# Kernel tuning notes

Measured on AMD Instinct MI355X. Metric: run time of the kernel, lower is better.

## Reference

```python
import jax, jax.numpy as jnp
import numpy as np

N_EMBD = 1024
N_HEAD = 16
HEAD_DIM = N_EMBD // N_HEAD
B, T = 2, 2048


def setup_inputs() -> dict:
    key = jax.random.key(0)
    ks = jax.random.split(key, 12)
    s = 0.02
    inp = {
        "x": jax.random.normal(ks[0], (B, T, N_EMBD), dtype=jnp.float32),
        "ln1_g": jnp.ones((N_EMBD,), jnp.float32),
        "ln1_b": jnp.zeros((N_EMBD,), jnp.float32),
        "ln2_g": jnp.ones((N_EMBD,), jnp.float32),
        "ln2_b": jnp.zeros((N_EMBD,), jnp.float32),
        "W_qkv": jax.random.normal(ks[1], (N_EMBD, 3 * N_EMBD), jnp.float32) * s,
        "b_qkv": jnp.zeros((3 * N_EMBD,), jnp.float32),
        "W_o": jax.random.normal(ks[2], (N_EMBD, N_EMBD), jnp.float32) * s,
        "b_o": jnp.zeros((N_EMBD,), jnp.float32),
        "W_fc": jax.random.normal(ks[3], (N_EMBD, 4 * N_EMBD), jnp.float32) * s,
        "b_fc": jnp.zeros((4 * N_EMBD,), jnp.float32),
        "W_proj": jax.random.normal(ks[4], (4 * N_EMBD, N_EMBD), jnp.float32) * s,
        "b_proj": jnp.zeros((N_EMBD,), jnp.float32),
    }
    return inp


def _layernorm(x, g, b, eps=1e-5):
    mu = jnp.mean(x, axis=-1, keepdims=True)
    var = jnp.var(x, axis=-1, keepdims=True)
    return (x - mu) * jax.lax.rsqrt(var + eps) * g + b


def _block(x, ln1_g, ln1_b, ln2_g, ln2_b, W_qkv, b_qkv, W_o, b_o, W_fc, b_fc, W_proj, b_proj):
    # --- attention sub-block (pre-LN) ---
    h = _layernorm(x, ln1_g, ln1_b)
    qkv = h @ W_qkv + b_qkv                     # [B,T,3E]
    q, k, v = jnp.split(qkv, 3, axis=-1)
    def split_heads(t):
        return t.reshape(B, T, N_HEAD, HEAD_DIM).transpose(0, 2, 1, 3)  # [B,H,T,D]
    q, k, v = split_heads(q), split_heads(k), split_heads(v)
    scores = jnp.einsum("bhqd,bhkd->bhqk", q, k) / (HEAD_DIM ** 0.5)
    causal = jnp.tril(jnp.ones((T, T), dtype=bool))
    scores = jnp.where(causal, scores, jnp.float32(-jnp.inf))
    probs = jax.nn.softmax(scores, axis=-1)
    attn = jnp.einsum("bhqk,bhkd->bhqd", probs, v)        # [B,H,T,D]
    attn = attn.transpose(0, 2, 1, 3).reshape(B, T, N_EMBD)
    x = x + attn @ W_o + b_o
    # --- MLP sub-block (pre-LN) ---
    h = _layernorm(x, ln2_g, ln2_b)
    h = jax.nn.gelu(h @ W_fc + b_fc, approximate=False)
    x = x + h @ W_proj + b_proj
    return x


def reference(x, ln1_g, ln1_b, ln2_g, ln2_b, W_qkv, b_qkv, W_o, b_o, W_fc, b_fc, W_proj, b_proj):
    return _block(x, ln1_g, ln1_b, ln2_g, ln2_b, W_qkv, b_qkv, W_o, b_o, W_fc, b_fc, W_proj, b_proj)
```

## Files before the change

### kernel.cpp

```cpp
#include <hip/hip_runtime.h>
#include <hip/hip_bf16.h>


#define TT 2048
#define EE 1024
#define NH 16
#define HD 64

#define AS1 __attribute__((address_space(1)))
#define AS3 __attribute__((address_space(3)))

using bf16x8 = __bf16 __attribute__((ext_vector_type(8)));
using bf16x4 = __bf16 __attribute__((ext_vector_type(4)));
using f32x4  = float __attribute__((ext_vector_type(4)));

template<int N> __device__ __forceinline__ void vm_wait() {
    if constexpr (N == 0)      asm volatile("s_waitcnt vmcnt(0)" ::: "memory");
    else if constexpr (N == 3) asm volatile("s_waitcnt vmcnt(3)" ::: "memory");
    else                       asm volatile("s_waitcnt vmcnt(4)" ::: "memory");
}

__device__ __forceinline__ float gelu_fast(float v) {
    float z  = v * 0.70710678118f;
    float az = fabsf(z);
    float t  = __builtin_amdgcn_rcpf(__builtin_fmaf(0.3275911f, az, 1.0f));
    float p  = t * __builtin_fmaf(t,
                   __builtin_fmaf(t,
                     __builtin_fmaf(t,
                       __builtin_fmaf(t, 1.061405429f, -1.453152027f),
                       1.421413741f),
                     -0.284496736f),
                   0.254829592f);
    float e  = __expf(-az * az);
    float er = copysignf(1.0f - p * e, z);
    return 0.5f * v * (1.0f + er);
}

__global__ __launch_bounds__(256) void convt_kernel(const float* __restrict__ W,
                                                    __bf16* __restrict__ WT,
                                                    int K, int N) {
    __shared__ __bf16 t[32][33];
    int n0 = blockIdx.x * 32, k0 = blockIdx.y * 32;
    int tid = threadIdx.x;
    int r = tid >> 3, c4 = (tid & 7) * 4;
    float4 v = *(const float4*)(W + (size_t)(k0 + r) * N + n0 + c4);
    t[r][c4 + 0] = (__bf16)v.x; t[r][c4 + 1] = (__bf16)v.y;
    t[r][c4 + 2] = (__bf16)v.z; t[r][c4 + 3] = (__bf16)v.w;
    __syncthreads();
    bf16x4 o;
    o[0] = t[c4 + 0][r]; o[1] = t[c4 + 1][r];
    o[2] = t[c4 + 2][r]; o[3] = t[c4 + 3][r];
    *(bf16x4*)(WT + (size_t)(n0 + r) * K + k0 + c4) = o;
}

__global__ __launch_bounds__(256) void ln_kernel(const float* __restrict__ x,
                                                 const float* __restrict__ g,
                                                 const float* __restrict__ bta,
                                                 __bf16* __restrict__ out) {
    int row = blockIdx.x;
    int tid = threadIdx.x;
    const float4 xv = *(const float4*)(x + (size_t)row * EE + tid * 4);
    float s  = xv.x + xv.y + xv.z + xv.w;
    float ss = xv.x*xv.x + xv.y*xv.y + xv.z*xv.z + xv.w*xv.w;
    __shared__ float rs[256], rss[256];
    rs[tid] = s; rss[tid] = ss;
    __syncthreads();
    for (int st = 128; st > 0; st >>= 1) {
        if (tid < st) { rs[tid] += rs[tid+st]; rss[tid] += rss[tid+st]; }
        __syncthreads();
    }
    float mean = rs[0] * (1.0f / EE);
    float var  = rss[0] * (1.0f / EE) - mean * mean;
    float rstd = rsqrtf(var + 1e-5f);
    const float4 gv = *(const float4*)(g + tid * 4);
    const float4 bv = *(const float4*)(bta + tid * 4);
    bf16x4 ov;
    ov[0] = (__bf16)((xv.x - mean) * rstd * gv.x + bv.x);
    ov[1] = (__bf16)((xv.y - mean) * rstd * gv.y + bv.y);
    ov[2] = (__bf16)((xv.z - mean) * rstd * gv.z + bv.z);
    ov[3] = (__bf16)((xv.w - mean) * rstd * gv.w + bv.w);
    *(bf16x4*)(out + (size_t)row * EE + tid * 4) = ov;
}

template<int TM, int TN, bool GELU, bool RESID, bool QKV, typename CT>
__global__ __launch_bounds__(256) void gemm_bt_kernel(const __bf16* __restrict__ A,
                                                      const __bf16* __restrict__ BT,
                                                      const float* __restrict__ bias,
                                                      const float* resid, CT* C,
                                                      __bf16* vT,
                                                      int M, int N, int K) {
    constexpr int MT = TM / 32;
    constexpr int NT = TN / 32;
    constexpr int LOADS = TM / 64 + TN / 64;
    __shared__ __align__(16) __bf16 As[3][TM][32];
    __shared__ __align__(16) __bf16 Bs[3][TN][32];
    int tid = threadIdx.x, wave = tid >> 6, lane = tid & 63;
    int quad = lane >> 4, l16 = lane & 15;
    int wm = wave >> 1, wn = wave & 1;
    int m0 = blockIdx.y * TM, n0 = blockIdx.x * TN;

    f32x4 acc[MT][NT] = {};

    int srow = wave * 16 + (lane >> 2);
    int scol = (lane & 3) * 8;

    auto STAGE = [&](int buf, int kt) {
        int kb = kt << 5;
#pragma unroll
        for (int p = 0; p < TM / 64; p++) {
            const __bf16* g = A + (size_t)(m0 + p * 64 + srow) * K + kb + scol;
            __builtin_amdgcn_global_load_lds((AS1 const void*)g,
                                             (AS3 void*)&As[buf][p * 64 + wave * 16][0],
                                             16, 0, 0);
        }
#pragma unroll
        for (int p = 0; p < TN / 64; p++) {
            const __bf16* g = BT + (size_t)(n0 + p * 64 + srow) * K + kb + scol;
            __builtin_amdgcn_global_load_lds((AS1 const void*)g,
                                             (AS3 void*)&Bs[buf][p * 64 + wave * 16][0],
                                             16, 0, 0);
        }
    };

    const int nk = K >> 5;
    STAGE(0, 0);
    STAGE(1, 1);
    vm_wait<LOADS>();
    __builtin_amdgcn_s_barrier();

    for (int t = 0; t < nk; ++t) {
        const int cur = t % 3;
        if (t + 2 < nk) STAGE((t + 2) % 3, t + 2);

        bf16x8 af[MT], bfr[NT];
#pragma unroll
        for (int mt = 0; mt < MT; mt++)
            af[mt] = *(const bf16x8*)(&As[cur][wm * (MT * 16) + mt * 16 + l16][quad * 8]);
#pragma unroll
        for (int nt = 0; nt < NT; nt++)
            bfr[nt] = *(const bf16x8*)(&Bs[cur][wn * (NT * 16) + nt * 16 + l16][quad * 8]);
#pragma unroll
        for (int mt = 0; mt < MT; mt++)
#pragma unroll
            for (int nt = 0; nt < NT; nt++)
                acc[mt][nt] = __builtin_amdgcn_mfma_f32_16x16x32_bf16(af[mt], bfr[nt],
                                                                      acc[mt][nt], 0, 0, 0);
        if (t + 1 < nk) {
            if (t + 2 < nk) vm_wait<LOADS>();
            else            vm_wait<0>();
            __builtin_amdgcn_s_barrier();
        }
    }

#pragma unroll
    for (int nt = 0; nt < NT; nt++) {
        int c = n0 + wn * (NT * 16) + nt * 16 + l16;
        float bv = bias[c];
#pragma unroll
        for (int mt = 0; mt < MT; mt++) {
#pragma unroll
            for (int r = 0; r < 4; r++) {
                int row = m0 + wm * (MT * 16) + mt * 16 + quad * 4 + r;
                float v = acc[mt][nt][r] + bv;
                if (GELU)  v = gelu_fast(v);
                if (RESID) v += resid[(size_t)row * N + c];
                if (!QKV) {
                    C[(size_t)row * N + c] = (CT)v;
                } else {
                    if (c < 2 * EE) {
                        ((__bf16*)C)[(size_t)row * (2 * EE) + c] = (__bf16)v;
                    } else {
                        int cv = c - 2 * EE;
                        int bb = row >> 11, t = row & (TT - 1);
                        vT[((size_t)(bb * NH + (cv >> 6)) * HD + (cv & 63)) * TT + t] =
                            (__bf16)v;
                    }
                }
            }
        }
    }
}

__global__ __launch_bounds__(256) void flash_attn_kernel(const __bf16* __restrict__ qkv,
                                                         const __bf16* __restrict__ vT,
                                                         __bf16* __restrict__ out) {
    int h = blockIdx.y, b = blockIdx.z;
    int tid = threadIdx.x, wave = tid >> 6, lane = tid & 63;
    int quad = lane >> 4, l16 = lane & 15;

    __shared__ __align__(16) __bf16 Ks[128 * 72];
    __shared__ __align__(16) __bf16 Ps[4][16 * 136];

    size_t base = (size_t)b * TT * (2 * EE);

    int srow = tid >> 3;
    int scol = (tid & 7) * 8;
    const __bf16* kbase  = qkv + base + EE + h * HD + scol;
    const __bf16* vrow = vT + (size_t)(b * NH + h) * HD * TT + (size_t)l16 * TT + quad * 8;
    __bf16* Psw = &Ps[wave][0];

    int nTiles = (int)gridDim.x * 2;

    for (int pass = 0; pass < 2; pass++) {
        int qt = pass == 0 ? (nTiles - 1 - blockIdx.x) : blockIdx.x;
        int q0 = qt * 64;

        int qrow = q0 + wave * 16 + l16;
        const __bf16* qp = qkv + base + (size_t)qrow * (2 * EE) + h * HD;
        bf16x8 aq0 = *(const bf16x8*)(qp + quad * 8);
        bf16x8 aq1 = *(const bf16x8*)(qp + 32 + quad * 8);

        f32x4 oacc[4] = {};
        float lsum[4] = {0.f, 0.f, 0.f, 0.f};
        int qg_base = q0 + wave * 16 + quad * 4;

        int nIter = (qt >> 1) + 1;

        bf16x8 kr[4];
#pragma unroll
        for (int p = 0; p < 4; p++)
            kr[p] = *(const bf16x8*)(kbase + (size_t)(32 * p + srow) * (2 * EE));

        for (int kt = 0; kt < nIter; ++kt) {
            int k0 = kt * 128;
#pragma unroll
            for (int p = 0; p < 4; p++)
                *(bf16x8*)(&Ks[(32 * p + srow) * 72 + scol]) = kr[p];
            __syncthreads();

            bf16x8 vf[4][4];
#pragma unroll
            for (int dt = 0; dt < 4; dt++)
#pragma unroll
                for (int w = 0; w < 4; w++)
                    vf[dt][w] = *(const bf16x8*)(vrow + (size_t)dt * (16 * TT) + k0 + w * 32);

            if (kt < nIter - 1) {
                int kn = k0 + 128;
#pragma unroll
                for (int p = 0; p < 4; p++)
                    kr[p] = *(const bf16x8*)(kbase + (size_t)(kn + 32 * p + srow) * (2 * EE));
            }

            f32x4 s[8];
#pragma unroll
            for (int nt = 0; nt < 8; nt++) {
                bf16x8 bk0 = *(const bf16x8*)(&Ks[(nt * 16 + l16) * 72 + quad * 8]);
                bf16x8 bk1 = *(const bf16x8*)(&Ks[(nt * 16 + l16) * 72 + 32 + quad * 8]);
                f32x4 z = {};
                z = __builtin_amdgcn_mfma_f32_16x16x32_bf16(aq0, bk0, z, 0, 0, 0);
                s[nt] = __builtin_amdgcn_mfma_f32_16x16x32_bf16(aq1, bk1, z, 0, 0, 0);
            }

            bool maskt = (kt == nIter - 1);
#pragma unroll
            for (int nt = 0; nt < 8; nt++) {
                int key = k0 + nt * 16 + l16;
                int cb = 2 * nt + (l16 >> 3);
#pragma unroll
                for (int r = 0; r < 4; r++) {
                    float p;
                    if (maskt && key > qg_base + r) p = 0.0f;
                    else p = __expf(fminf(s[nt][r] * 0.125f, 30.0f));
                    lsum[r] += p;
                    int q = quad * 4 + r;
                    int col = (((cb & 8) | ((cb - 2 * q) & 7)) << 3) | (l16 & 7);
                    Psw[q * 136 + col] = (__bf16)p;
                }
            }

#pragma unroll
            for (int w = 0; w < 4; w++) {
                int cbr = 4 * w + quad;
                int colr = ((cbr & 8) | ((cbr - 2 * l16) & 7)) << 3;
                bf16x8 ap = *(const bf16x8*)(&Psw[l16 * 136 + colr]);
#pragma unroll
                for (int dt = 0; dt < 4; dt++)
                    oacc[dt] = __builtin_amdgcn_mfma_f32_16x16x32_bf16(ap, vf[dt][w],
                                                                       oacc[dt], 0, 0, 0);
            }
            __syncthreads();
        }

#pragma unroll
        for (int off = 1; off < 16; off <<= 1)
#pragma unroll
            for (int r = 0; r < 4; r++) lsum[r] += __shfl_xor(lsum[r], off);
#pragma unroll
        for (int dt = 0; dt < 4; dt++) {
#pragma unroll
            for (int r = 0; r < 4; r++) {
                int qg = qg_base + r;
                out[((size_t)b * TT + qg) * EE + h * HD + dt * 16 + l16] =
                    (__bf16)(oacc[dt][r] / lsum[r]);
            }
        }
    }
}

extern "C" void kernel_launch(void* const* d_in, const int* in_sizes, int n_in,
                              void* d_out, int out_size, void* d_ws, size_t ws_size,
                              hipStream_t stream) {
    const float* x     = (const float*)d_in[0];
    const float* ln1g  = (const float*)d_in[1];
    const float* ln1b  = (const float*)d_in[2];
    const float* ln2g  = (const float*)d_in[3];
    const float* ln2b  = (const float*)d_in[4];
    const float* Wqkv  = (const float*)d_in[5];
    const float* bqkv  = (const float*)d_in[6];
    const float* Wo    = (const float*)d_in[7];
    const float* bo    = (const float*)d_in[8];
    const float* Wfc   = (const float*)d_in[9];
    const float* bfc   = (const float*)d_in[10];
    const float* Wproj = (const float*)d_in[11];
    const float* bproj = (const float*)d_in[12];
    float* out = (float*)d_out;

    const int M = 2 * TT;

    __bf16* ws = (__bf16*)d_ws;
    __bf16* regQ   = ws;
    __bf16* regS   = ws + 16777216;
    __bf16* WfcT   = ws + 20971520;
    __bf16* qkv    = regQ;
    __bf16* vT     = regQ + 8388608;
    __bf16* WqkvT  = regQ + 12582912;
    __bf16* WoT    = regQ + 15728640;
    __bf16* ff     = regQ;
    __bf16* h1 = regS, *atn = regS, *h2 = regS;
    __bf16* WprojT = regS;
    float*  x1 = out;

    convt_kernel<<<dim3(3 * EE / 32, EE / 32), 256, 0, stream>>>(Wqkv, WqkvT, EE, 3 * EE);
    convt_kernel<<<dim3(EE / 32, EE / 32), 256, 0, stream>>>(Wo, WoT, EE, EE);
    convt_kernel<<<dim3(4 * EE / 32, EE / 32), 256, 0, stream>>>(Wfc, WfcT, EE, 4 * EE);

    ln_kernel<<<M, 256, 0, stream>>>(x, ln1g, ln1b, h1);
    gemm_bt_kernel<128, 128, false, false, true, __bf16>
        <<<dim3(3 * EE / 128, M / 128), 256, 0, stream>>>(
        h1, WqkvT, bqkv, nullptr, qkv, vT, M, 3 * EE, EE);
    flash_attn_kernel<<<dim3(TT / 128, NH, 2), 256, 0, stream>>>(qkv, vT, atn);
    gemm_bt_kernel<128, 64, false, true, false, float>
        <<<dim3(EE / 64, M / 128), 256, 0, stream>>>(
        atn, WoT, bo, x, x1, nullptr, M, EE, EE);
    ln_kernel<<<M, 256, 0, stream>>>(x1, ln2g, ln2b, h2);
    gemm_bt_kernel<128, 128, true, false, false, __bf16>
        <<<dim3(4 * EE / 128, M / 128), 256, 0, stream>>>(
        h2, WfcT, bfc, nullptr, ff, nullptr, M, 4 * EE, EE);
    convt_kernel<<<dim3(EE / 32, 4 * EE / 32), 256, 0, stream>>>(Wproj, WprojT, 4 * EE, EE);
    gemm_bt_kernel<128, 64, false, true, false, float>
        <<<dim3(EE / 64, M / 128), 256, 0, stream>>>(
        ff, WprojT, bproj, x1, out, nullptr, M, EE, 4 * EE);
}
```

Measured before the change: 429.3 us.

## Deepen GEMM LDS pipeline to four stages and XOR-swizzle LDS tiles

The bf16 GEMM kernel now uses four shared-memory buffers, prefetching three k-tiles ahead, whenever each stage issues three or fewer loads. The vmcnt wait thresholds are derived from the pipeline depth, and a separate tail loop drains the remaining tiles. Global-to-LDS copies and the fragment reads now use a matching XOR swizzle on the 16-byte column chunk, meant to reduce LDS bank conflicts on the bf16x8 reads. The extra buffer raises LDS use per block, which may lower occupancy.

```diff
diff --git a/kernel.cpp b/kernel.cpp
--- a/kernel.cpp
+++ b/kernel.cpp
@@ -16,8 +16,11 @@
 
 template<int N> __device__ __forceinline__ void vm_wait() {
     if constexpr (N == 0)      asm volatile("s_waitcnt vmcnt(0)" ::: "memory");
+    else if constexpr (N == 2) asm volatile("s_waitcnt vmcnt(2)" ::: "memory");
     else if constexpr (N == 3) asm volatile("s_waitcnt vmcnt(3)" ::: "memory");
-    else                       asm volatile("s_waitcnt vmcnt(4)" ::: "memory");
+    else if constexpr (N == 4) asm volatile("s_waitcnt vmcnt(4)" ::: "memory");
+    else if constexpr (N == 6) asm volatile("s_waitcnt vmcnt(6)" ::: "memory");
+    else                       asm volatile("s_waitcnt vmcnt(8)" ::: "memory");
 }
 
 __device__ __forceinline__ float gelu_fast(float v) {
@@ -92,8 +95,11 @@
     constexpr int MT = TM / 32;
     constexpr int NT = TN / 32;
     constexpr int LOADS = TM / 64 + TN / 64;
-    __shared__ __align__(16) __bf16 As[3][TM][32];
-    __shared__ __align__(16) __bf16 Bs[3][TN][32];
+    constexpr int NBUF  = (LOADS <= 3) ? 4 : 3;
+    constexpr int DEPTH = NBUF - 1;
+    constexpr int WAITN = (DEPTH - 1) * LOADS;
+    __shared__ __align__(16) __bf16 As[NBUF][TM][32];
+    __shared__ __align__(16) __bf16 Bs[NBUF][TN][32];
     int tid = threadIdx.x, wave = tid >> 6, lane = tid & 63;
     int quad = lane >> 4, l16 = lane & 15;
     int wm = wave >> 1, wn = wave & 1;
@@ -102,7 +108,8 @@
     f32x4 acc[MT][NT] = {};
 
     int srow = wave * 16 + (lane >> 2);
-    int scol = (lane & 3) * 8;
+    int scol = (((lane & 3) ^ ((lane >> 3) & 3)) * 8);
+    int xcol = ((quad ^ ((l16 >> 1) & 3)) * 8);
 
     auto STAGE = [&](int buf, int kt) {
         int kb = kt << 5;
@@ -122,32 +129,41 @@
         }
     };
 
-    const int nk = K >> 5;
-    STAGE(0, 0);
-    STAGE(1, 1);
-    vm_wait<LOADS>();
-    __builtin_amdgcn_s_barrier();
-
-    for (int t = 0; t < nk; ++t) {
-        const int cur = t % 3;
-        if (t + 2 < nk) STAGE((t + 2) % 3, t + 2);
-
+    auto COMPUTE = [&](int cur) {
         bf16x8 af[MT], bfr[NT];
 #pragma unroll
         for (int mt = 0; mt < MT; mt++)
-            af[mt] = *(const bf16x8*)(&As[cur][wm * (MT * 16) + mt * 16 + l16][quad * 8]);
+            af[mt] = *(const bf16x8*)(&As[cur][wm * (MT * 16) + mt * 16 + l16][xcol]);
 #pragma unroll
         for (int nt = 0; nt < NT; nt++)
-            bfr[nt] = *(const bf16x8*)(&Bs[cur][wn * (NT * 16) + nt * 16 + l16][quad * 8]);
+            bfr[nt] = *(const bf16x8*)(&Bs[cur][wn * (NT * 16) + nt * 16 + l16][xcol]);
 #pragma unroll
         for (int mt = 0; mt < MT; mt++)
 #pragma unroll
             for (int nt = 0; nt < NT; nt++)
                 acc[mt][nt] = __builtin_amdgcn_mfma_f32_16x16x32_bf16(af[mt], bfr[nt],
                                                                       acc[mt][nt], 0, 0, 0);
+    };
+
+    const int nk = K >> 5;
+#pragma unroll
+    for (int i = 0; i < DEPTH; ++i) STAGE(i, i);
+    vm_wait<WAITN>();
+    __builtin_amdgcn_s_barrier();
+
+    int t = 0;
+    for (; t + DEPTH < nk; ++t) {
+        STAGE((t + DEPTH) % NBUF, t + DEPTH);
+        COMPUTE(t % NBUF);
+        vm_wait<WAITN>();
+        __builtin_amdgcn_s_barrier();
+    }
+    for (; t < nk; ++t) {
+        COMPUTE(t % NBUF);
         if (t + 1 < nk) {
-            if (t + 2 < nk) vm_wait<LOADS>();
-            else            vm_wait<0>();
+            int rem = nk - 2 - t;
+            if (rem >= 1) vm_wait<LOADS>();
+            else          vm_wait<0>();
             __builtin_amdgcn_s_barrier();
         }
     }
@@ -171,8 +187,8 @@
                         ((__bf16*)C)[(size_t)row * (2 * EE) + c] = (__bf16)v;
                     } else {
                         int cv = c - 2 * EE;
-                        int bb = row >> 11, t = row & (TT - 1);
-                        vT[((size_t)(bb * NH + (cv >> 6)) * HD + (cv & 63)) * TT + t] =
+                        int bb = row >> 11, tt = row & (TT - 1);
+                        vT[((size_t)(bb * NH + (cv >> 6)) * HD + (cv & 63)) * TT + tt] =
                             (__bf16)v;
                     }
                 }
```

Result: no change. 426.9 us (-0.5%).
